# Kernel optimization log

Measured on AMD Instinct MI355X. Metric: run time of the kernel, lower is better.

## Reference

```python
import jax, jax.numpy as jnp
import numpy as np

B, S, D = 4, 2048, 1024
EPS = 1e-6


def setup_inputs() -> dict:
    key = jax.random.key(0)
    ks = jax.random.split(key, 9)
    s = 1.0 / np.sqrt(D)
    return {
        "context": jax.random.normal(ks[0], (B, S, D), jnp.float32),
        "eos_mask": jax.random.randint(ks[1], (B, S, S), 0, 2, dtype=jnp.int32),
        "prior": jax.random.uniform(ks[2], (B, S, S), jnp.float32),
        "Wq": jax.random.uniform(ks[3], (D, D), jnp.float32, -s, s),
        "bq": jax.random.uniform(ks[4], (D,), jnp.float32, -s, s),
        "Wk": jax.random.uniform(ks[5], (D, D), jnp.float32, -s, s),
        "bk": jax.random.uniform(ks[6], (D,), jnp.float32, -s, s),
        "gamma": jnp.ones((D,), jnp.float32),
        "beta": jnp.zeros((D,), jnp.float32),
    }


def reference(context, eos_mask, prior, Wq, bq, Wk, bk, gamma, beta):
    d = context.shape[-1]
    seq = context.shape[1]

    # LayerNorm with torch's unbiased std (Bessel correction)
    mean = jnp.mean(context, axis=-1, keepdims=True)
    var = jnp.sum((context - mean) ** 2, axis=-1, keepdims=True) / (d - 1)
    x = gamma * (context - mean) / (jnp.sqrt(var) + EPS) + beta

    q = x @ Wq + bq  # linear_query
    k = x @ Wk + bk  # linear_key

    scores = jnp.einsum("bid,bjd->bij", q, k) / d  # note: /d, not /sqrt(d)

    idx = jnp.arange(seq)
    band = jnp.abs(idx[:, None] - idx[None, :]) == 1      # a + c (tridiagonal off-diagonals)
    sup = (idx[None, :] - idx[:, None]) == 1              # a (superdiagonal)
    strict_upper = idx[:, None] < idx[None, :]            # triu(ones) - eye
    eye = idx[:, None] == idx[None, :]

    mask = (eos_mask != 0) & band[None]                   # eos_mask & (a + c)
    scores = jnp.where(mask, scores, -1e9)
    na = jax.nn.softmax(scores, axis=-1)
    na = jnp.sqrt(na * jnp.swapaxes(na, -1, -2) + 1e-9)
    na = prior + (1.0 - prior) * na                       # hier_add_index branch

    # t = log(na+eps).masked_fill(a==0,0) @ triu  ==  cumsum along last axis
    t = jnp.where(sup[None], jnp.log(na + 1e-9), 0.0)
    t = jnp.cumsum(t, axis=-1)
    # g = triu @ t  ==  reversed cumsum along axis -2
    g = jnp.cumsum(t[..., ::-1, :], axis=-2)[..., ::-1, :]
    g = jnp.where(strict_upper[None], jnp.exp(g), 0.0)

    g_attn = g + jnp.swapaxes(g, -1, -2) + jnp.where(eye[None], na, 1e-9)
    return (g_attn, na)
```

## Files before the change

kernel.cpp:

```cpp
#include <hip/hip_runtime.h>
#include <hip/hip_bf16.h>
#include <cmath>

#define BB 4
#define SS 2048
#define DD 1024
#define BS (BB*SS)
constexpr float EPS = 1e-6f;

typedef __attribute__((ext_vector_type(8))) short short8;
typedef __attribute__((ext_vector_type(4))) float floatx4;

__device__ inline float bf2f(unsigned short u) {
    unsigned v = ((unsigned)u) << 16;
    float f; __builtin_memcpy(&f, &v, 4);
    return f;
}

__global__ __launch_bounds__(256)
void prep_kernel(const float* __restrict__ Wq, const float* __restrict__ Wk,
                 const float* __restrict__ bq, const float* __restrict__ bk,
                 __hip_bfloat16* __restrict__ Wb, float* __restrict__ u,
                 float* __restrict__ v, float* __restrict__ cs,
                 float* __restrict__ sacc) {
    int blk = blockIdx.x;
    if (blk < 2048) {
        int idx = blk * 256 + threadIdx.x;
        const int half = DD * DD / 4;
        const float* src = (idx < half) ? Wk : Wq;
        int off = (idx < half) ? idx : idx - half;
        float4 val = ((const float4*)src)[off];
        union { ushort4 uu; __hip_bfloat16 h[4]; } pk;
        pk.h[0] = __float2bfloat16(val.x);
        pk.h[1] = __float2bfloat16(val.y);
        pk.h[2] = __float2bfloat16(val.z);
        pk.h[3] = __float2bfloat16(val.w);
        ((ushort4*)Wb)[idx] = pk.uu;
    } else if (blk < 2561) {
        int gid = (blk - 2048) * 4 + (threadIdx.x >> 6);
        int lane = threadIdx.x & 63;
        if (gid > 2048) return;
        const float* row; const float* vec; float* outp;
        if (gid < 1024)      { row = Wq + (size_t)gid * DD;          vec = bk; outp = u + gid; }
        else if (gid < 2048) { row = Wk + (size_t)(gid - 1024) * DD; vec = bq; outp = v + (gid - 1024); }
        else                 { row = bq;                             vec = bk; outp = cs; }
        float s = 0.f;
        #pragma unroll
        for (int k = 0; k < 4; ++k) {
            float4 a = ((const float4*)row)[lane * 4 + k];
            float4 b = ((const float4*)vec)[lane * 4 + k];
            s += a.x * b.x + a.y * b.y + a.z * b.z + a.w * b.w;
        }
        #pragma unroll
        for (int off = 32; off; off >>= 1) s += __shfl_down(s, off);
        if (lane == 0) *outp = s;
    } else {
        int idx = (blk - 2561) * 1024 + threadIdx.x * 4;
        *(float4*)(sacc + idx) = make_float4(0.f, 0.f, 0.f, 0.f);
    }
}

__global__ __launch_bounds__(256)
void ln_kernel(const float* __restrict__ ctx, const float* __restrict__ gamma,
               const float* __restrict__ beta, const float* __restrict__ u,
               const float* __restrict__ v, const float* __restrict__ cs,
               __hip_bfloat16* __restrict__ xo, float* __restrict__ alpha,
               float* __restrict__ betav) {
    int row = blockIdx.x;
    int t = threadIdx.x;
    const float* r = ctx + (size_t)row * DD;
    float4 val = ((const float4*)r)[t];
    float s1 = val.x + val.y + val.z + val.w;
    float s2 = val.x*val.x + val.y*val.y + val.z*val.z + val.w*val.w;
    #pragma unroll
    for (int off = 32; off; off >>= 1) {
        s1 += __shfl_down(s1, off);
        s2 += __shfl_down(s2, off);
    }
    __shared__ float ls1[4], ls2[4];
    int wid = t >> 6, lane = t & 63;
    if (lane == 0) { ls1[wid] = s1; ls2[wid] = s2; }
    __syncthreads();
    if (t == 0) {
        float a = ls1[0] + ls1[1] + ls1[2] + ls1[3];
        float b = ls2[0] + ls2[1] + ls2[2] + ls2[3];
        float mean = a / DD;
        float var = (b - a * a / DD) / (DD - 1);
        ls1[0] = mean;
        ls2[0] = 1.0f / (sqrtf(var) + EPS);
    }
    __syncthreads();
    float mean = ls1[0], rstd = ls2[0];
    float4 g = ((const float4*)gamma)[t];
    float4 be = ((const float4*)beta)[t];
    float nx0 = g.x * (val.x - mean) * rstd + be.x;
    float nx1 = g.y * (val.y - mean) * rstd + be.y;
    float nx2 = g.z * (val.z - mean) * rstd + be.z;
    float nx3 = g.w * (val.w - mean) * rstd + be.w;
    union { ushort4 uu; __hip_bfloat16 h[4]; } pk;
    pk.h[0] = __float2bfloat16(nx0);
    pk.h[1] = __float2bfloat16(nx1);
    pk.h[2] = __float2bfloat16(nx2);
    pk.h[3] = __float2bfloat16(nx3);
    ((ushort4*)(xo + (size_t)row * DD))[t] = pk.uu;
    float4 u4 = ((const float4*)u)[t];
    float4 v4 = ((const float4*)v)[t];
    float du = nx0 * u4.x + nx1 * u4.y + nx2 * u4.z + nx3 * u4.w;
    float dv = nx0 * v4.x + nx1 * v4.y + nx2 * v4.z + nx3 * v4.w;
    #pragma unroll
    for (int off = 32; off; off >>= 1) {
        du += __shfl_down(du, off);
        dv += __shfl_down(dv, off);
    }
    __syncthreads();
    if (lane == 0) { ls1[wid] = du; ls2[wid] = dv; }
    __syncthreads();
    if (t == 0) {
        alpha[row] = ls1[0] + ls1[1] + ls1[2] + ls1[3] + *cs;
        betav[row] = ls2[0] + ls2[1] + ls2[2] + ls2[3];
    }
}

__global__ __launch_bounds__(256)
void gemm64_mfma(const __hip_bfloat16* __restrict__ A,
                 const __hip_bfloat16* __restrict__ B,
                 __hip_bfloat16* __restrict__ C, int ldc) {
    __shared__ short As[64 * 64];
    __shared__ short Bs[64 * 64];
    int tid = threadIdx.x;
    int wave = tid >> 6;
    int lane = tid & 63;
    int q = lane >> 4, m16 = lane & 15;
    int srow = lane >> 3;
    int skoff = ((lane & 7) ^ srow) * 8;

    const __hip_bfloat16* gA = A + ((size_t)blockIdx.x * 64 + wave * 16 + srow) * DD + skoff;
    const __hip_bfloat16* gB = B + ((size_t)blockIdx.y * 64 + wave * 16 + srow) * DD + skoff;
    short* lA0 = As + (wave * 16) * 64;
    short* lA1 = As + (wave * 16 + 8) * 64;
    short* lB0 = Bs + (wave * 16) * 64;
    short* lB1 = Bs + (wave * 16 + 8) * 64;

    int swr = (m16 & 7) * 8;

    floatx4 acc[4] = {};
    for (int k0 = 0; k0 < DD; k0 += 64) {
        __builtin_amdgcn_global_load_lds(
            (const __attribute__((address_space(1))) void*)(gA + k0),
            (__attribute__((address_space(3))) void*)(lA0), 16, 0, 0);
        __builtin_amdgcn_global_load_lds(
            (const __attribute__((address_space(1))) void*)(gA + k0 + 8 * DD),
            (__attribute__((address_space(3))) void*)(lA1), 16, 0, 0);
        __builtin_amdgcn_global_load_lds(
            (const __attribute__((address_space(1))) void*)(gB + k0),
            (__attribute__((address_space(3))) void*)(lB0), 16, 0, 0);
        __builtin_amdgcn_global_load_lds(
            (const __attribute__((address_space(1))) void*)(gB + k0 + 8 * DD),
            (__attribute__((address_space(3))) void*)(lB1), 16, 0, 0);
        __syncthreads();
        #pragma unroll
        for (int h = 0; h < 2; ++h) {
            short8 af = *(const short8*)(As + (wave * 16 + m16) * 64 + ((h * 32 + q * 8) ^ swr));
            #pragma unroll
            for (int c = 0; c < 4; ++c) {
                short8 bf_ = *(const short8*)(Bs + (c * 16 + m16) * 64 + ((h * 32 + q * 8) ^ swr));
                acc[c] = __builtin_amdgcn_mfma_f32_16x16x32_bf16(af, bf_, acc[c], 0, 0, 0);
            }
        }
        __syncthreads();
    }
    #pragma unroll
    for (int c = 0; c < 4; ++c) {
        int gcol = blockIdx.y * 64 + c * 16 + m16;
        #pragma unroll
        for (int e = 0; e < 4; ++e) {
            int grow = blockIdx.x * 64 + wave * 16 + q * 4 + e;
            C[(size_t)grow * ldc + gcol] = __float2bfloat16(acc[c][e]);
        }
    }
}

#define TM 128
#define TN 128
#define BK 64
__global__ __launch_bounds__(256)
void gemm2_fused(const __hip_bfloat16* __restrict__ A,
                 const __hip_bfloat16* __restrict__ B,
                 float* __restrict__ sacc) {
    __shared__ short smem[32768];
    int tid = threadIdx.x;
    int wave = tid >> 6;
    int lane = tid & 63;
    int wm = wave >> 1, wn = wave & 1;
    int q = lane >> 4, m16 = lane & 15;

    int srow = lane >> 3;
    int skoff = ((lane & 7) ^ srow) * 8;
    const __hip_bfloat16* gA = A + ((size_t)blockIdx.x * TM + wave * 32 + srow) * DD + skoff;
    const __hip_bfloat16* gB = B + ((size_t)blockIdx.y * TN + wave * 32 + srow) * DD + skoff;

    int swr = (m16 & 7) * 8;

    floatx4 acc[4][4] = {};

    #define STAGE(p, k0) do {                                                        \
        short* As_ = smem + (p) * 16384;                                             \
        short* Bs_ = As_ + 8192;                                                     \
        _Pragma("unroll")                                                            \
        for (int i_ = 0; i_ < 4; ++i_) {                                             \
            __builtin_amdgcn_global_load_lds(                                        \
                (const __attribute__((address_space(1))) void*)(gA + (k0) + i_ * 8 * DD), \
                (__attribute__((address_space(3))) void*)(As_ + (wave * 32 + i_ * 8) * BK), 16, 0, 0); \
            __builtin_amdgcn_global_load_lds(                                        \
                (const __attribute__((address_space(1))) void*)(gB + (k0) + i_ * 8 * DD), \
                (__attribute__((address_space(3))) void*)(Bs_ + (wave * 32 + i_ * 8) * BK), 16, 0, 0); \
        }                                                                            \
    } while (0)

    #define COMPUTE(p) do {                                                          \
        const short* As_ = smem + (p) * 16384;                                       \
        const short* Bs_ = As_ + 8192;                                               \
        _Pragma("unroll")                                                            \
        for (int kk = 0; kk < 2; ++kk) {                                             \
            short8 af[4], bfr[4];                                                    \
            _Pragma("unroll")                                                        \
            for (int r = 0; r < 4; ++r)                                              \
                af[r] = *(const short8*)(As_ + (wm * 64 + r * 16 + m16) * BK + ((kk * 32 + q * 8) ^ swr)); \
            _Pragma("unroll")                                                        \
            for (int c = 0; c < 4; ++c)                                              \
                bfr[c] = *(const short8*)(Bs_ + (wn * 64 + c * 16 + m16) * BK + ((kk * 32 + q * 8) ^ swr)); \
            _Pragma("unroll")                                                        \
            for (int r = 0; r < 4; ++r)                                              \
                _Pragma("unroll")                                                    \
                for (int c = 0; c < 4; ++c)                                          \
                    acc[r][c] = __builtin_amdgcn_mfma_f32_16x16x32_bf16(af[r], bfr[c], acc[r][c], 0, 0, 0); \
        }                                                                            \
    } while (0)

    STAGE(0, 0);
    __syncthreads();
    for (int t = 0; t < DD / BK; t += 2) {
        if (t + 1 < DD / BK) STAGE(1, (t + 1) * BK);
        COMPUTE(0);
        __syncthreads();
        if (t + 2 < DD / BK) STAGE(0, (t + 2) * BK);
        COMPUTE(1);
        __syncthreads();
    }
    #undef STAGE
    #undef COMPUTE

    short* EP = smem + wave * 4608;
    #pragma unroll
    for (int r = 0; r < 4; ++r)
        #pragma unroll
        for (int c = 0; c < 4; ++c)
            #pragma unroll
            for (int e = 0; e < 4; ++e) {
                __hip_bfloat16 hv = __float2bfloat16(acc[r][c][e]);
                EP[(r * 16 + q * 4 + e) * 72 + c * 16 + m16] = *(short*)&hv;
            }

    int rl = lane;
    int growZ = blockIdx.x * TM + wm * 64 + rl;
    int gcol0 = blockIdx.y * TN + wn * 64;
    bool hs = (growZ + 1 < BS);
    bool hb = (growZ >= 1);
    const short8* psup = (const short8*)(A + (size_t)(growZ + 1) * DD + gcol0);
    const short8* psub = (const short8*)(A + (size_t)(growZ - 1) * DD + gcol0);
    float sup = 0.f, sub = 0.f;
    #pragma unroll
    for (int c8 = 0; c8 < 8; ++c8) {
        short8 zz = *(const short8*)(EP + rl * 72 + c8 * 8);
        float zf[8];
        #pragma unroll
        for (int e = 0; e < 8; ++e) zf[e] = bf2f((unsigned short)zz[e]);
        if (hs) {
            short8 xx = psup[c8];
            #pragma unroll
            for (int e = 0; e < 8; ++e) sup += zf[e] * bf2f((unsigned short)xx[e]);
        }
        if (hb) {
            short8 xx = psub[c8];
            #pragma unroll
            for (int e = 0; e < 8; ++e) sub += zf[e] * bf2f((unsigned short)xx[e]);
        }
    }
    if (hs) atomicAdd(&sacc[growZ], sup);
    if (hb) atomicAdd(&sacc[BS + growZ], sub);
}

__global__ __launch_bounds__(256)
void softmax_kernel(const float* __restrict__ sacc, const int* __restrict__ eos,
                    const float* __restrict__ alpha, const float* __restrict__ betav,
                    float* __restrict__ vsub, float* __restrict__ vsup,
                    float* __restrict__ wuni) {
    int gw = blockIdx.x * 256 + threadIdx.x;
    int i = gw & (SS - 1);
    float a = alpha[gw];
    float ssup = 0.f, ssub = 0.f;
    if (i < SS - 1) ssup = (sacc[gw] + a + betav[gw + 1]) * (1.0f / DD);
    if (i > 0)      ssub = (sacc[BS + gw] + a + betav[gw - 1]) * (1.0f / DD);
    bool msub = (i > 0) && (eos[(size_t)gw * SS + (i - 1)] != 0);
    bool msup = (i < SS - 1) && (eos[(size_t)gw * SS + (i + 1)] != 0);
    float vs, vp, w;
    if (msub && msup) {
        float mx = fmaxf(ssub, ssup);
        float e1 = expf(ssub - mx), e2 = expf(ssup - mx);
        float inv = 1.0f / (e1 + e2);
        vs = e1 * inv; vp = e2 * inv; w = 0.f;
    } else if (msub) { vs = 1.f; vp = 0.f; w = 0.f; }
    else if (msup)   { vs = 0.f; vp = 1.f; w = 0.f; }
    else             { vs = vp = w = 1.0f / SS; }
    vsub[gw] = vs; vsup[gw] = vp; wuni[gw] = w;
}

__global__ __launch_bounds__(256)
void scan_kernel(const float* __restrict__ prior, const float* __restrict__ vsub,
                 const float* __restrict__ vsup, double* __restrict__ Lc) {
    int b = blockIdx.x;
    int t = threadIdx.x;
    double loc[8];
    double s = 0.0;
    #pragma unroll
    for (int k = 0; k < 8; ++k) {
        int tt = t * 8 + k;
        double Lv = 0.0;
        if (tt < SS - 1) {
            float pr = prior[((size_t)(b * SS + tt)) * SS + tt + 1];
            float na2 = sqrtf(vsup[b * SS + tt] * vsub[b * SS + tt + 1] + 1e-9f);
            float P = pr + (1.f - pr) * na2;
            Lv = log((double)P + 1e-9);
        }
        loc[k] = Lv; s += Lv;
    }
    __shared__ double sa[256], sb[256];
    sa[t] = s;
    __syncthreads();
    double* src = sa; double* dst = sb;
    for (int off = 1; off < 256; off <<= 1) {
        double v = src[t];
        if (t >= off) v += src[t - off];
        __syncthreads();
        dst[t] = v;
        __syncthreads();
        double* tmp = src; src = dst; dst = tmp;
    }
    double run = (t == 0) ? 0.0 : src[t - 1];
    #pragma unroll
    for (int k = 0; k < 8; ++k) {
        int idx = t * 8 + k;
        Lc[b * SS + idx] = run;
        run += loc[k];
    }
}

__global__ __launch_bounds__(256)
void out_kernel(const float* __restrict__ prior, const float* __restrict__ vsub,
                const float* __restrict__ vsup, const float* __restrict__ wuni,
                const double* __restrict__ Lc, float* __restrict__ out_g,
                float* __restrict__ out_na) {
    size_t gid = (size_t)blockIdx.x * 256 + threadIdx.x;
    int jt = (int)(gid & 511);
    int row = (int)(gid >> 9);
    int i = row & (SS - 1);
    int b = row >> 11;
    int j0 = jt * 4;
    size_t base = (size_t)row * SS + j0;
    float4 pr4 = *(const float4*)(prior + base);
    float4 wj4 = *(const float4*)(wuni + b * SS + j0);
    float pra[4] = {pr4.x, pr4.y, pr4.z, pr4.w};
    float wja[4] = {wj4.x, wj4.y, wj4.z, wj4.w};
    float wi = wuni[row];
    double Lci = Lc[row];
    const double* Lcb = Lc + b * SS;
    float nav[4], gv[4];
    #pragma unroll
    for (int c = 0; c < 4; ++c) {
        int j = j0 + c;
        float prod;
        if (j == i - 1)      prod = vsub[row] * vsup[row - 1];
        else if (j == i + 1) prod = vsup[row] * vsub[row + 1];
        else if (j == i)     prod = wi * wi;
        else                 prod = wi * wja[c];
        float na2 = sqrtf(prod + 1e-9f);
        float p = pra[c];
        float na3 = p + (1.f - p) * na2;
        nav[c] = na3;
        if (j == i) {
            gv[c] = na3;
        } else {
            double d = (j > i) ? (Lcb[j] - Lci) : (Lci - Lcb[j]);
            gv[c] = expf((float)d) + 1e-9f;
        }
    }
    *(float4*)(out_g + base) = make_float4(gv[0], gv[1], gv[2], gv[3]);
    *(float4*)(out_na + base) = make_float4(nav[0], nav[1], nav[2], nav[3]);
}

extern "C" void kernel_launch(void* const* d_in, const int* in_sizes, int n_in,
                              void* d_out, int out_size, void* d_ws, size_t ws_size,
                              hipStream_t stream) {
    const float* ctx   = (const float*)d_in[0];
    const int*   eos   = (const int*)d_in[1];
    const float* prior = (const float*)d_in[2];
    const float* Wq    = (const float*)d_in[3];
    const float* bq    = (const float*)d_in[4];
    const float* Wk    = (const float*)d_in[5];
    const float* bk    = (const float*)d_in[6];
    const float* gamma = (const float*)d_in[7];
    const float* beta  = (const float*)d_in[8];

    float* out_g  = (float*)d_out;
    float* out_na = out_g + (size_t)BB * SS * SS;

    char* ws = (char*)d_ws;
    size_t o = 0;
    __hip_bfloat16* x  = (__hip_bfloat16*)(ws + o); o += (size_t)BS * DD * 2;
    __hip_bfloat16* Wb = (__hip_bfloat16*)(ws + o); o += (size_t)2 * DD * DD * 2;
    __hip_bfloat16* Mt = (__hip_bfloat16*)(ws + o); o += (size_t)DD * DD * 2;
    double* Lc   = (double*)(ws + o); o += (size_t)BS * 8;
    float* u     = (float*)(ws + o);  o += DD * 4;
    float* v     = (float*)(ws + o);  o += DD * 4;
    float* cs    = (float*)(ws + o);  o += 64;
    float* alpha = (float*)(ws + o);  o += (size_t)BS * 4;
    float* betav = (float*)(ws + o);  o += (size_t)BS * 4;
    float* vsub  = (float*)(ws + o);  o += (size_t)BS * 4;
    float* vsup  = (float*)(ws + o);  o += (size_t)BS * 4;
    float* wuni  = (float*)(ws + o);  o += (size_t)BS * 4;
    float* sacc  = (float*)(ws + o);  o += (size_t)2 * BS * 4;

    __hip_bfloat16* Wk_bf = Wb;
    __hip_bfloat16* Wq_bf = Wb + (size_t)DD * DD;

    prep_kernel<<<2577, 256, 0, stream>>>(Wq, Wk, bq, bk, Wb, u, v, cs, sacc);
    ln_kernel<<<BS, 256, 0, stream>>>(ctx, gamma, beta, u, v, cs, x, alpha, betav);

    dim3 g1(DD / 64, DD / 64);
    gemm64_mfma<<<g1, 256, 0, stream>>>(Wk_bf, Wq_bf, Mt, DD);

    dim3 g2(BS / TM, DD / TN);
    gemm2_fused<<<g2, 256, 0, stream>>>(x, Mt, sacc);

    softmax_kernel<<<BS / 256, 256, 0, stream>>>(sacc, eos, alpha, betav, vsub, vsup, wuni);

    scan_kernel<<<BB, 256, 0, stream>>>(prior, vsub, vsup, Lc);

    size_t total = (size_t)BB * SS * SS / 4;
    out_kernel<<<(int)(total / 256), 256, 0, stream>>>(prior, vsub, vsup, wuni, Lc,
                                                       out_g, out_na);
}
```

Measured before the change: 321.1 us.

## Merge LN with weight GEMM, fuse softmax into scan, grid-stride output kernel

The LayerNorm blocks and the Wk·Wq^T GEMM blocks now run as one launch by splitting on block index, so the two independent stages can overlap and one launch is saved. The per-row softmax is folded into the per-batch scan kernel, which now uses 512 threads and 4 elements per thread, removing another launch. The output kernel uses a grid-stride loop with 8 iterations per thread over a fixed 2048-block grid. The fused post kernel runs only 4 blocks, so the softmax work, including its strided eos gathers, is serialized onto very few CUs.

```diff
diff --git a/kernel.cpp b/kernel.cpp
--- a/kernel.cpp
+++ b/kernel.cpp
@@ -61,121 +61,125 @@
 }
 
 __global__ __launch_bounds__(256)
-void ln_kernel(const float* __restrict__ ctx, const float* __restrict__ gamma,
-               const float* __restrict__ beta, const float* __restrict__ u,
-               const float* __restrict__ v, const float* __restrict__ cs,
-               __hip_bfloat16* __restrict__ xo, float* __restrict__ alpha,
-               float* __restrict__ betav) {
-    int row = blockIdx.x;
+void ln_gemm_kernel(const float* __restrict__ ctx, const float* __restrict__ gamma,
+                    const float* __restrict__ beta, const float* __restrict__ u,
+                    const float* __restrict__ v, const float* __restrict__ cs,
+                    __hip_bfloat16* __restrict__ xo, float* __restrict__ alpha,
+                    float* __restrict__ betav,
+                    const __hip_bfloat16* __restrict__ Wk_bf,
+                    const __hip_bfloat16* __restrict__ Wq_bf,
+                    __hip_bfloat16* __restrict__ Mt) {
+    __shared__ short shmem[8192];
     int t = threadIdx.x;
-    const float* r = ctx + (size_t)row * DD;
-    float4 val = ((const float4*)r)[t];
-    float s1 = val.x + val.y + val.z + val.w;
-    float s2 = val.x*val.x + val.y*val.y + val.z*val.z + val.w*val.w;
-    #pragma unroll
-    for (int off = 32; off; off >>= 1) {
-        s1 += __shfl_down(s1, off);
-        s2 += __shfl_down(s2, off);
-    }
-    __shared__ float ls1[4], ls2[4];
-    int wid = t >> 6, lane = t & 63;
-    if (lane == 0) { ls1[wid] = s1; ls2[wid] = s2; }
-    __syncthreads();
-    if (t == 0) {
-        float a = ls1[0] + ls1[1] + ls1[2] + ls1[3];
-        float b = ls2[0] + ls2[1] + ls2[2] + ls2[3];
-        float mean = a / DD;
-        float var = (b - a * a / DD) / (DD - 1);
-        ls1[0] = mean;
-        ls2[0] = 1.0f / (sqrtf(var) + EPS);
-    }
-    __syncthreads();
-    float mean = ls1[0], rstd = ls2[0];
-    float4 g = ((const float4*)gamma)[t];
-    float4 be = ((const float4*)beta)[t];
-    float nx0 = g.x * (val.x - mean) * rstd + be.x;
-    float nx1 = g.y * (val.y - mean) * rstd + be.y;
-    float nx2 = g.z * (val.z - mean) * rstd + be.z;
-    float nx3 = g.w * (val.w - mean) * rstd + be.w;
-    union { ushort4 uu; __hip_bfloat16 h[4]; } pk;
-    pk.h[0] = __float2bfloat16(nx0);
-    pk.h[1] = __float2bfloat16(nx1);
-    pk.h[2] = __float2bfloat16(nx2);
-    pk.h[3] = __float2bfloat16(nx3);
-    ((ushort4*)(xo + (size_t)row * DD))[t] = pk.uu;
-    float4 u4 = ((const float4*)u)[t];
-    float4 v4 = ((const float4*)v)[t];
-    float du = nx0 * u4.x + nx1 * u4.y + nx2 * u4.z + nx3 * u4.w;
-    float dv = nx0 * v4.x + nx1 * v4.y + nx2 * v4.z + nx3 * v4.w;
-    #pragma unroll
-    for (int off = 32; off; off >>= 1) {
-        du += __shfl_down(du, off);
-        dv += __shfl_down(dv, off);
-    }
-    __syncthreads();
-    if (lane == 0) { ls1[wid] = du; ls2[wid] = dv; }
-    __syncthreads();
-    if (t == 0) {
-        alpha[row] = ls1[0] + ls1[1] + ls1[2] + ls1[3] + *cs;
-        betav[row] = ls2[0] + ls2[1] + ls2[2] + ls2[3];
-    }
-}
-
-__global__ __launch_bounds__(256)
-void gemm64_mfma(const __hip_bfloat16* __restrict__ A,
-                 const __hip_bfloat16* __restrict__ B,
-                 __hip_bfloat16* __restrict__ C, int ldc) {
-    __shared__ short As[64 * 64];
-    __shared__ short Bs[64 * 64];
-    int tid = threadIdx.x;
-    int wave = tid >> 6;
-    int lane = tid & 63;
-    int q = lane >> 4, m16 = lane & 15;
-    int srow = lane >> 3;
-    int skoff = ((lane & 7) ^ srow) * 8;
-
-    const __hip_bfloat16* gA = A + ((size_t)blockIdx.x * 64 + wave * 16 + srow) * DD + skoff;
-    const __hip_bfloat16* gB = B + ((size_t)blockIdx.y * 64 + wave * 16 + srow) * DD + skoff;
-    short* lA0 = As + (wave * 16) * 64;
-    short* lA1 = As + (wave * 16 + 8) * 64;
-    short* lB0 = Bs + (wave * 16) * 64;
-    short* lB1 = Bs + (wave * 16 + 8) * 64;
-
-    int swr = (m16 & 7) * 8;
-
-    floatx4 acc[4] = {};
-    for (int k0 = 0; k0 < DD; k0 += 64) {
-        __builtin_amdgcn_global_load_lds(
-            (const __attribute__((address_space(1))) void*)(gA + k0),
-            (__attribute__((address_space(3))) void*)(lA0), 16, 0, 0);
-        __builtin_amdgcn_global_load_lds(
-            (const __attribute__((address_space(1))) void*)(gA + k0 + 8 * DD),
-            (__attribute__((address_space(3))) void*)(lA1), 16, 0, 0);
-        __builtin_amdgcn_global_load_lds(
-            (const __attribute__((address_space(1))) void*)(gB + k0),
-            (__attribute__((address_space(3))) void*)(lB0), 16, 0, 0);
-        __builtin_amdgcn_global_load_lds(
-            (const __attribute__((address_space(1))) void*)(gB + k0 + 8 * DD),
-            (__attribute__((address_space(3))) void*)(lB1), 16, 0, 0);
-        __syncthreads();
-        #pragma unroll
-        for (int h = 0; h < 2; ++h) {
-            short8 af = *(const short8*)(As + (wave * 16 + m16) * 64 + ((h * 32 + q * 8) ^ swr));
+
+    if (blockIdx.x < 8192) {
+        int row = blockIdx.x;
+        float* ls1 = (float*)shmem;
+        float* ls2 = ls1 + 4;
+        const float* r = ctx + (size_t)row * DD;
+        float4 val = ((const float4*)r)[t];
+        float s1 = val.x + val.y + val.z + val.w;
+        float s2 = val.x*val.x + val.y*val.y + val.z*val.z + val.w*val.w;
+        #pragma unroll
+        for (int off = 32; off; off >>= 1) {
+            s1 += __shfl_down(s1, off);
+            s2 += __shfl_down(s2, off);
+        }
+        int wid = t >> 6, lane = t & 63;
+        if (lane == 0) { ls1[wid] = s1; ls2[wid] = s2; }
+        __syncthreads();
+        if (t == 0) {
+            float a = ls1[0] + ls1[1] + ls1[2] + ls1[3];
+            float b = ls2[0] + ls2[1] + ls2[2] + ls2[3];
+            float mean = a / DD;
+            float var = (b - a * a / DD) / (DD - 1);
+            ls1[0] = mean;
+            ls2[0] = 1.0f / (sqrtf(var) + EPS);
+        }
+        __syncthreads();
+        float mean = ls1[0], rstd = ls2[0];
+        float4 g = ((const float4*)gamma)[t];
+        float4 be = ((const float4*)beta)[t];
+        float nx0 = g.x * (val.x - mean) * rstd + be.x;
+        float nx1 = g.y * (val.y - mean) * rstd + be.y;
+        float nx2 = g.z * (val.z - mean) * rstd + be.z;
+        float nx3 = g.w * (val.w - mean) * rstd + be.w;
+        union { ushort4 uu; __hip_bfloat16 h[4]; } pk;
+        pk.h[0] = __float2bfloat16(nx0);
+        pk.h[1] = __float2bfloat16(nx1);
+        pk.h[2] = __float2bfloat16(nx2);
+        pk.h[3] = __float2bfloat16(nx3);
+        ((ushort4*)(xo + (size_t)row * DD))[t] = pk.uu;
+        float4 u4 = ((const float4*)u)[t];
+        float4 v4 = ((const float4*)v)[t];
+        float du = nx0 * u4.x + nx1 * u4.y + nx2 * u4.z + nx3 * u4.w;
+        float dv = nx0 * v4.x + nx1 * v4.y + nx2 * v4.z + nx3 * v4.w;
+        #pragma unroll
+        for (int off = 32; off; off >>= 1) {
+            du += __shfl_down(du, off);
+            dv += __shfl_down(dv, off);
+        }
+        __syncthreads();
+        if (lane == 0) { ls1[wid] = du; ls2[wid] = dv; }
+        __syncthreads();
+        if (t == 0) {
+            alpha[row] = ls1[0] + ls1[1] + ls1[2] + ls1[3] + *cs;
+            betav[row] = ls2[0] + ls2[1] + ls2[2] + ls2[3];
+        }
+    } else {
+        int bx = blockIdx.x - 8192;
+        int gx = bx & 15, gy = bx >> 4;
+        short* As = shmem;
+        short* Bs = shmem + 4096;
+        int wave = t >> 6;
+        int lane = t & 63;
+        int q = lane >> 4, m16 = lane & 15;
+        int srow = lane >> 3;
+        int skoff = ((lane & 7) ^ srow) * 8;
+
+        const __hip_bfloat16* gA = Wk_bf + ((size_t)gx * 64 + wave * 16 + srow) * DD + skoff;
+        const __hip_bfloat16* gB = Wq_bf + ((size_t)gy * 64 + wave * 16 + srow) * DD + skoff;
+        short* lA0 = As + (wave * 16) * 64;
+        short* lA1 = As + (wave * 16 + 8) * 64;
+        short* lB0 = Bs + (wave * 16) * 64;
+        short* lB1 = Bs + (wave * 16 + 8) * 64;
+
+        int swr = (m16 & 7) * 8;
+
+        floatx4 acc[4] = {};
+        for (int k0 = 0; k0 < DD; k0 += 64) {
+            __builtin_amdgcn_global_load_lds(
+                (const __attribute__((address_space(1))) void*)(gA + k0),
+                (__attribute__((address_space(3))) void*)(lA0), 16, 0, 0);
+            __builtin_amdgcn_global_load_lds(
+                (const __attribute__((address_space(1))) void*)(gA + k0 + 8 * DD),
+                (__attribute__((address_space(3))) void*)(lA1), 16, 0, 0);
+            __builtin_amdgcn_global_load_lds(
+                (const __attribute__((address_space(1))) void*)(gB + k0),
+                (__attribute__((address_space(3))) void*)(lB0), 16, 0, 0);
+            __builtin_amdgcn_global_load_lds(
+                (const __attribute__((address_space(1))) void*)(gB + k0 + 8 * DD),
+                (__attribute__((address_space(3))) void*)(lB1), 16, 0, 0);
+            __syncthreads();
             #pragma unroll
-            for (int c = 0; c < 4; ++c) {
-                short8 bf_ = *(const short8*)(Bs + (c * 16 + m16) * 64 + ((h * 32 + q * 8) ^ swr));
-                acc[c] = __builtin_amdgcn_mfma_f32_16x16x32_bf16(af, bf_, acc[c], 0, 0, 0);
+            for (int h = 0; h < 2; ++h) {
+                short8 af = *(const short8*)(As + (wave * 16 + m16) * 64 + ((h * 32 + q * 8) ^ swr));
+                #pragma unroll
+                for (int c = 0; c < 4; ++c) {
+                    short8 bf_ = *(const short8*)(Bs + (c * 16 + m16) * 64 + ((h * 32 + q * 8) ^ swr));
+                    acc[c] = __builtin_amdgcn_mfma_f32_16x16x32_bf16(af, bf_, acc[c], 0, 0, 0);
+                }
             }
-        }
-        __syncthreads();
-    }
-    #pragma unroll
-    for (int c = 0; c < 4; ++c) {
-        int gcol = blockIdx.y * 64 + c * 16 + m16;
-        #pragma unroll
-        for (int e = 0; e < 4; ++e) {
-            int grow = blockIdx.x * 64 + wave * 16 + q * 4 + e;
-            C[(size_t)grow * ldc + gcol] = __float2bfloat16(acc[c][e]);
+            __syncthreads();
+        }
+        #pragma unroll
+        for (int c = 0; c < 4; ++c) {
+            int gcol = gy * 64 + c * 16 + m16;
+            #pragma unroll
+            for (int e = 0; e < 4; ++e) {
+                int grow = gx * 64 + wave * 16 + q * 4 + e;
+                Mt[(size_t)grow * DD + gcol] = __float2bfloat16(acc[c][e]);
+            }
         }
     }
 }
@@ -290,41 +294,41 @@
     if (hb) atomicAdd(&sacc[BS + growZ], sub);
 }
 
-__global__ __launch_bounds__(256)
-void softmax_kernel(const float* __restrict__ sacc, const int* __restrict__ eos,
-                    const float* __restrict__ alpha, const float* __restrict__ betav,
-                    float* __restrict__ vsub, float* __restrict__ vsup,
-                    float* __restrict__ wuni) {
-    int gw = blockIdx.x * 256 + threadIdx.x;
-    int i = gw & (SS - 1);
-    float a = alpha[gw];
-    float ssup = 0.f, ssub = 0.f;
-    if (i < SS - 1) ssup = (sacc[gw] + a + betav[gw + 1]) * (1.0f / DD);
-    if (i > 0)      ssub = (sacc[BS + gw] + a + betav[gw - 1]) * (1.0f / DD);
-    bool msub = (i > 0) && (eos[(size_t)gw * SS + (i - 1)] != 0);
-    bool msup = (i < SS - 1) && (eos[(size_t)gw * SS + (i + 1)] != 0);
-    float vs, vp, w;
-    if (msub && msup) {
-        float mx = fmaxf(ssub, ssup);
-        float e1 = expf(ssub - mx), e2 = expf(ssup - mx);
-        float inv = 1.0f / (e1 + e2);
-        vs = e1 * inv; vp = e2 * inv; w = 0.f;
-    } else if (msub) { vs = 1.f; vp = 0.f; w = 0.f; }
-    else if (msup)   { vs = 0.f; vp = 1.f; w = 0.f; }
-    else             { vs = vp = w = 1.0f / SS; }
-    vsub[gw] = vs; vsup[gw] = vp; wuni[gw] = w;
-}
-
-__global__ __launch_bounds__(256)
-void scan_kernel(const float* __restrict__ prior, const float* __restrict__ vsub,
-                 const float* __restrict__ vsup, double* __restrict__ Lc) {
+__global__ __launch_bounds__(512)
+void post_kernel(const float* __restrict__ sacc, const int* __restrict__ eos,
+                 const float* __restrict__ alpha, const float* __restrict__ betav,
+                 const float* __restrict__ prior,
+                 float* __restrict__ vsub, float* __restrict__ vsup,
+                 float* __restrict__ wuni, double* __restrict__ Lc) {
     int b = blockIdx.x;
     int t = threadIdx.x;
-    double loc[8];
+    #pragma unroll
+    for (int k = 0; k < 4; ++k) {
+        int i = t + 512 * k;
+        int gw = b * SS + i;
+        float a = alpha[gw];
+        float ssup = 0.f, ssub = 0.f;
+        if (i < SS - 1) ssup = (sacc[gw] + a + betav[gw + 1]) * (1.0f / DD);
+        if (i > 0)      ssub = (sacc[BS + gw] + a + betav[gw - 1]) * (1.0f / DD);
+        bool msub = (i > 0) && (eos[(size_t)gw * SS + (i - 1)] != 0);
+        bool msup = (i < SS - 1) && (eos[(size_t)gw * SS + (i + 1)] != 0);
+        float vs, vp, w;
+        if (msub && msup) {
+            float mx = fmaxf(ssub, ssup);
+            float e1 = expf(ssub - mx), e2 = expf(ssup - mx);
+            float inv = 1.0f / (e1 + e2);
+            vs = e1 * inv; vp = e2 * inv; w = 0.f;
+        } else if (msub) { vs = 1.f; vp = 0.f; w = 0.f; }
+        else if (msup)   { vs = 0.f; vp = 1.f; w = 0.f; }
+        else             { vs = vp = w = 1.0f / SS; }
+        vsub[gw] = vs; vsup[gw] = vp; wuni[gw] = w;
+    }
+    __syncthreads();
+    double loc[4];
     double s = 0.0;
     #pragma unroll
-    for (int k = 0; k < 8; ++k) {
-        int tt = t * 8 + k;
+    for (int k = 0; k < 4; ++k) {
+        int tt = t * 4 + k;
         double Lv = 0.0;
         if (tt < SS - 1) {
             float pr = prior[((size_t)(b * SS + tt)) * SS + tt + 1];
@@ -334,11 +338,11 @@
         }
         loc[k] = Lv; s += Lv;
     }
-    __shared__ double sa[256], sb[256];
+    __shared__ double sa[512], sb[512];
     sa[t] = s;
     __syncthreads();
     double* src = sa; double* dst = sb;
-    for (int off = 1; off < 256; off <<= 1) {
+    for (int off = 1; off < 512; off <<= 1) {
         double v = src[t];
         if (t >= off) v += src[t - off];
         __syncthreads();
@@ -348,8 +352,8 @@
     }
     double run = (t == 0) ? 0.0 : src[t - 1];
     #pragma unroll
-    for (int k = 0; k < 8; ++k) {
-        int idx = t * 8 + k;
+    for (int k = 0; k < 4; ++k) {
+        int idx = t * 4 + k;
         Lc[b * SS + idx] = run;
         run += loc[k];
     }
@@ -360,42 +364,46 @@
                 const float* __restrict__ vsup, const float* __restrict__ wuni,
                 const double* __restrict__ Lc, float* __restrict__ out_g,
                 float* __restrict__ out_na) {
+    const size_t stride = (size_t)2048 * 256;
     size_t gid = (size_t)blockIdx.x * 256 + threadIdx.x;
-    int jt = (int)(gid & 511);
-    int row = (int)(gid >> 9);
-    int i = row & (SS - 1);
-    int b = row >> 11;
-    int j0 = jt * 4;
-    size_t base = (size_t)row * SS + j0;
-    float4 pr4 = *(const float4*)(prior + base);
-    float4 wj4 = *(const float4*)(wuni + b * SS + j0);
-    float pra[4] = {pr4.x, pr4.y, pr4.z, pr4.w};
-    float wja[4] = {wj4.x, wj4.y, wj4.z, wj4.w};
-    float wi = wuni[row];
-    double Lci = Lc[row];
-    const double* Lcb = Lc + b * SS;
-    float nav[4], gv[4];
-    #pragma unroll
-    for (int c = 0; c < 4; ++c) {
-        int j = j0 + c;
-        float prod;
-        if (j == i - 1)      prod = vsub[row] * vsup[row - 1];
-        else if (j == i + 1) prod = vsup[row] * vsub[row + 1];
-        else if (j == i)     prod = wi * wi;
-        else                 prod = wi * wja[c];
-        float na2 = sqrtf(prod + 1e-9f);
-        float p = pra[c];
-        float na3 = p + (1.f - p) * na2;
-        nav[c] = na3;
-        if (j == i) {
-            gv[c] = na3;
-        } else {
-            double d = (j > i) ? (Lcb[j] - Lci) : (Lci - Lcb[j]);
-            gv[c] = expf((float)d) + 1e-9f;
-        }
-    }
-    *(float4*)(out_g + base) = make_float4(gv[0], gv[1], gv[2], gv[3]);
-    *(float4*)(out_na + base) = make_float4(nav[0], nav[1], nav[2], nav[3]);
+    #pragma unroll
+    for (int it = 0; it < 8; ++it, gid += stride) {
+        int jt = (int)(gid & 511);
+        int row = (int)(gid >> 9);
+        int i = row & (SS - 1);
+        int b = row >> 11;
+        int j0 = jt * 4;
+        size_t base = (size_t)row * SS + j0;
+        float4 pr4 = *(const float4*)(prior + base);
+        float4 wj4 = *(const float4*)(wuni + b * SS + j0);
+        float pra[4] = {pr4.x, pr4.y, pr4.z, pr4.w};
+        float wja[4] = {wj4.x, wj4.y, wj4.z, wj4.w};
+        float wi = wuni[row];
+        double Lci = Lc[row];
+        const double* Lcb = Lc + b * SS;
+        float nav[4], gv[4];
+        #pragma unroll
+        for (int c = 0; c < 4; ++c) {
+            int j = j0 + c;
+            float prod;
+            if (j == i - 1)      prod = vsub[row] * vsup[row - 1];
+            else if (j == i + 1) prod = vsup[row] * vsub[row + 1];
+            else if (j == i)     prod = wi * wi;
+            else                 prod = wi * wja[c];
+            float na2 = sqrtf(prod + 1e-9f);
+            float p = pra[c];
+            float na3 = p + (1.f - p) * na2;
+            nav[c] = na3;
+            if (j == i) {
+                gv[c] = na3;
+            } else {
+                double d = (j > i) ? (Lcb[j] - Lci) : (Lci - Lcb[j]);
+                gv[c] = expf((float)d) + 1e-9f;
+            }
+        }
+        *(float4*)(out_g + base) = make_float4(gv[0], gv[1], gv[2], gv[3]);
+        *(float4*)(out_na + base) = make_float4(nav[0], nav[1], nav[2], nav[3]);
+    }
 }
 
 extern "C" void kernel_launch(void* const* d_in, const int* in_sizes, int n_in,
@@ -434,19 +442,16 @@
     __hip_bfloat16* Wq_bf = Wb + (size_t)DD * DD;
 
     prep_kernel<<<2577, 256, 0, stream>>>(Wq, Wk, bq, bk, Wb, u, v, cs, sacc);
-    ln_kernel<<<BS, 256, 0, stream>>>(ctx, gamma, beta, u, v, cs, x, alpha, betav);
-
-    dim3 g1(DD / 64, DD / 64);
-    gemm64_mfma<<<g1, 256, 0, stream>>>(Wk_bf, Wq_bf, Mt, DD);
+
+    ln_gemm_kernel<<<8448, 256, 0, stream>>>(ctx, gamma, beta, u, v, cs,
+                                             x, alpha, betav, Wk_bf, Wq_bf, Mt);
 
     dim3 g2(BS / TM, DD / TN);
     gemm2_fused<<<g2, 256, 0, stream>>>(x, Mt, sacc);
 
-    softmax_kernel<<<BS / 256, 256, 0, stream>>>(sacc, eos, alpha, betav, vsub, vsup, wuni);
-
-    scan_kernel<<<BB, 256, 0, stream>>>(prior, vsub, vsup, Lc);
-
-    size_t total = (size_t)BB * SS * SS / 4;
-    out_kernel<<<(int)(total / 256), 256, 0, stream>>>(prior, vsub, vsup, wuni, Lc,
-                                                       out_g, out_na);
-}
+    post_kernel<<<BB, 512, 0, stream>>>(sacc, eos, alpha, betav, prior,
+                                        vsub, vsup, wuni, Lc);
+
+    out_kernel<<<2048, 256, 0, stream>>>(prior, vsub, vsup, wuni, Lc,
+                                         out_g, out_na);
+}
```

Result: slower. 338.3 us (+5.4%).
